# Kernel optimization log

Measured on AMD Instinct MI355X. Metric: run time of the kernel, lower is better.

## Reference

```python
import jax, jax.numpy as jnp
import numpy as np


def setup_inputs() -> dict:
    key = jax.random.key(0)
    k1, k2 = jax.random.split(key)
    B, C, H, W, T = 64, 128, 8, 8, 100
    outputs = jax.random.normal(k1, (B, C, H, W, T), dtype=jnp.float32)
    target = jax.random.uniform(k2, (B, C, H, W, T), dtype=jnp.float32)
    return {"outputs": outputs, "target": target, "n_steps": T, "tau_s": 2}


def _psp(x, tau_s):
    # x: [B, C, H, W, T]; fixed-coefficient leaky integrator over last axis.
    # syn_t = syn_{t-1} * (1 - 1/tau_s) + x_t ; out_t = syn_t / tau_s
    decay = 1.0 - 1.0 / tau_s
    xt = jnp.moveaxis(x, -1, 0)  # [T, B, C, H, W]

    def step(syn, x_t):
        syn = syn * decay + x_t
        return syn, syn / tau_s

    syn0 = jnp.zeros(x.shape[:-1], dtype=x.dtype)
    _, syns = jax.lax.scan(step, syn0, xt)
    return jnp.moveaxis(syns, 0, -1)  # [B, C, H, W, T]


def reference(outputs, target, n_steps, tau_s):
    # n_steps is implied by the trailing axis; kept for signature fidelity.
    target_psp = _psp(target, float(tau_s))
    delta = outputs - target_psp
    return 0.5 * jnp.sum(delta * delta)
```

## Files before the change

kernel.cpp:

```cpp
#include <hip/hip_runtime.h>


constexpr int T    = 100;
constexpr int SEG  = 25;
constexpr int PIX  = 32;
constexpr int TF   = PIX * T;
constexpr int FULL = (TF * 4) / 1024;

typedef const __attribute__((address_space(1))) void* gas_t;
typedef __attribute__((address_space(3))) void*       las_t;

__global__ __launch_bounds__(128) void spike_loss_kernel(
    const float* __restrict__ tgt,
    const float* __restrict__ outs,
    const int*   __restrict__ tau_p,
    float*       __restrict__ out,
    int n_tiles, int tiles_per_block)
{
    __shared__ float lds_t[2][TF];
    __shared__ float lds_o[2][TF];
    __shared__ float ws[2];

    const float tau     = (float)tau_p[0];
    const float inv_tau = 1.0f / tau;
    const float decay   = 1.0f - inv_tau;
    float d25 = 1.0f;
    #pragma unroll
    for (int i = 0; i < SEG; ++i) d25 *= decay;
    const float d50 = d25 * d25;

    const int lane = threadIdx.x & 63;
    const int wv   = threadIdx.x >> 6;

    const int first = blockIdx.x * tiles_per_block;
    int cnt = n_tiles - first;
    if (cnt < 0) cnt = 0;
    if (cnt > tiles_per_block) cnt = tiles_per_block;

    float acc = 0.0f;

    auto stage = [&](int tile, int buf) {
        const float* gt = tgt  + (size_t)tile * TF;
        const float* go = outs + (size_t)tile * TF;
        #pragma unroll
        for (int i = 0; i < FULL / 2; ++i) {
            const int c   = i * 2 + wv;
            const int off = c * 256 + lane * 4;
            __builtin_amdgcn_global_load_lds((gas_t)(gt + off),
                (las_t)&lds_t[buf][c * 256], 16, 0, 0);
            __builtin_amdgcn_global_load_lds((gas_t)(go + off),
                (las_t)&lds_o[buf][c * 256], 16, 0, 0);
        }
        {
            const int off = FULL * 256 + wv * 64 + lane;
            __builtin_amdgcn_global_load_lds((gas_t)(gt + off),
                (las_t)&lds_t[buf][FULL * 256 + wv * 64], 4, 0, 0);
            __builtin_amdgcn_global_load_lds((gas_t)(go + off),
                (las_t)&lds_o[buf][FULL * 256 + wv * 64], 4, 0, 0);
        }
    };

    auto process = [&](int buf) {
        const int p    = threadIdx.x >> 2;
        const int q    = threadIdx.x & 3;
        const int base = p * T + q * SEG;

        float s[SEG];
        float syn = 0.0f;
        #pragma unroll
        for (int i = 0; i < SEG; ++i) {
            syn = fmaf(syn, decay, lds_t[buf][base + i]);
            s[i] = syn;
        }
        const float f1 = __shfl_up(syn, 1, 64);
        const float f2 = __shfl_up(syn, 2, 64);
        const float f3 = __shfl_up(syn, 3, 64);
        float carry = (q >= 1) ? f1 : 0.0f;
        if (q >= 2) carry = fmaf(f2, d25, carry);
        if (q >= 3) carry = fmaf(f3, d50, carry);

        float cp = carry;
        #pragma unroll
        for (int i = 0; i < SEG; ++i) {
            cp *= decay;
            const float st = s[i] + cp;
            const float d  = fmaf(st, -inv_tau, lds_o[buf][base + i]);
            acc = fmaf(d, d, acc);
        }
    };

    if (cnt > 0) stage(first, 0);

    for (int k = 0; k < cnt; ++k) {
        asm volatile("s_waitcnt vmcnt(0)" ::: "memory");
        __syncthreads();
        if (k + 1 < cnt) stage(first + k + 1, (k + 1) & 1);
        process(k & 1);
    }

    #pragma unroll
    for (int off = 32; off > 0; off >>= 1)
        acc += __shfl_down(acc, off, 64);
    if (lane == 0) ws[wv] = acc;
    __syncthreads();
    if (threadIdx.x == 0)
        atomicAdd(out, 0.5f * (ws[0] + ws[1]));
}

extern "C" void kernel_launch(void* const* d_in, const int* in_sizes, int n_in,
                              void* d_out, int out_size, void* d_ws, size_t ws_size,
                              hipStream_t stream) {
    const float* outs = (const float*)d_in[0];
    const float* tgt  = (const float*)d_in[1];
    const int* tau_p  = (const int*)d_in[3];
    float* out        = (float*)d_out;

    const int n_pixels = in_sizes[0] / T;
    const int n_tiles  = n_pixels / PIX;

    const int block = 128;
    const int grid  = 768;
    const int tiles_per_block = (n_tiles + grid - 1) / grid;

    hipMemsetAsync(out, 0, sizeof(float), stream);

    spike_loss_kernel<<<grid, block, 0, stream>>>(
        tgt, outs, tau_p, out, n_tiles, tiles_per_block);
}
```

Measured before the change: 413.3 us.

## Use single-wave blocks, stage only target in LDS, load outputs directly

```diff
diff --git a/kernel.cpp b/kernel.cpp
--- a/kernel.cpp
+++ b/kernel.cpp
@@ -1,25 +1,25 @@
 #include <hip/hip_runtime.h>
 
 
-constexpr int T    = 100;
-constexpr int SEG  = 25;
-constexpr int PIX  = 32;
-constexpr int TF   = PIX * T;
-constexpr int FULL = (TF * 4) / 1024;
+constexpr int T   = 100;
+constexpr int SEG = 25;
+constexpr int PIX = 16;
+constexpr int TF  = PIX * T;
+constexpr int NCH = (TF * 4) / 1024;
+constexpr int NV4 = TF / 4;
 
 typedef const __attribute__((address_space(1))) void* gas_t;
 typedef __attribute__((address_space(3))) void*       las_t;
+typedef float f4 __attribute__((ext_vector_type(4)));
 
-__global__ __launch_bounds__(128) void spike_loss_kernel(
+__global__ __launch_bounds__(64) void spike_loss_kernel(
     const float* __restrict__ tgt,
     const float* __restrict__ outs,
     const int*   __restrict__ tau_p,
     float*       __restrict__ out,
     int n_tiles, int tiles_per_block)
 {
-    __shared__ float lds_t[2][TF];
-    __shared__ float lds_o[2][TF];
-    __shared__ float ws[2];
+    __shared__ __align__(16) float lds_t[2][TF];
 
     const float tau     = (float)tau_p[0];
     const float inv_tau = 1.0f / tau;
@@ -29,40 +29,30 @@
     for (int i = 0; i < SEG; ++i) d25 *= decay;
     const float d50 = d25 * d25;
 
-    const int lane = threadIdx.x & 63;
-    const int wv   = threadIdx.x >> 6;
+    const int tid = threadIdx.x;
 
     const int first = blockIdx.x * tiles_per_block;
     int cnt = n_tiles - first;
     if (cnt < 0) cnt = 0;
     if (cnt > tiles_per_block) cnt = tiles_per_block;
+    if (cnt <= 0) return;
 
     float acc = 0.0f;
 
     auto stage = [&](int tile, int buf) {
-        const float* gt = tgt  + (size_t)tile * TF;
-        const float* go = outs + (size_t)tile * TF;
+        const float* gt = tgt + (size_t)tile * TF;
         #pragma unroll
-        for (int i = 0; i < FULL / 2; ++i) {
-            const int c   = i * 2 + wv;
-            const int off = c * 256 + lane * 4;
-            __builtin_amdgcn_global_load_lds((gas_t)(gt + off),
+        for (int c = 0; c < NCH; ++c) {
+            __builtin_amdgcn_global_load_lds((gas_t)(gt + c * 256 + tid * 4),
                 (las_t)&lds_t[buf][c * 256], 16, 0, 0);
-            __builtin_amdgcn_global_load_lds((gas_t)(go + off),
-                (las_t)&lds_o[buf][c * 256], 16, 0, 0);
         }
-        {
-            const int off = FULL * 256 + wv * 64 + lane;
-            __builtin_amdgcn_global_load_lds((gas_t)(gt + off),
-                (las_t)&lds_t[buf][FULL * 256 + wv * 64], 4, 0, 0);
-            __builtin_amdgcn_global_load_lds((gas_t)(go + off),
-                (las_t)&lds_o[buf][FULL * 256 + wv * 64], 4, 0, 0);
-        }
+        __builtin_amdgcn_global_load_lds((gas_t)(gt + NCH * 256 + tid),
+            (las_t)&lds_t[buf][NCH * 256], 4, 0, 0);
     };
 
     auto process = [&](int buf) {
-        const int p    = threadIdx.x >> 2;
-        const int q    = threadIdx.x & 3;
+        const int p    = tid >> 2;
+        const int q    = tid & 3;
         const int base = p * T + q * SEG;
 
         float s[SEG];
@@ -83,28 +73,56 @@
         #pragma unroll
         for (int i = 0; i < SEG; ++i) {
             cp *= decay;
-            const float st = s[i] + cp;
-            const float d  = fmaf(st, -inv_tau, lds_o[buf][base + i]);
-            acc = fmaf(d, d, acc);
+            lds_t[buf][base + i] = s[i] + cp;
         }
     };
 
-    if (cnt > 0) stage(first, 0);
+    auto pass2 = [&](int tile, int buf) {
+        const f4* o4 = (const f4*)(outs + (size_t)tile * TF);
+        const f4* p4 = (const f4*)lds_t[buf];
+        #pragma unroll
+        for (int j = 0; j < NV4 / 64; ++j) {
+            const int idx = tid + 64 * j;
+            const f4 o = o4[idx];
+            const f4 sy = p4[idx];
+            #pragma unroll
+            for (int c = 0; c < 4; ++c) {
+                const float d = fmaf(sy[c], -inv_tau, o[c]);
+                acc = fmaf(d, d, acc);
+            }
+        }
+        if (tid < NV4 - (NV4 / 64) * 64) {
+            const int idx = (NV4 / 64) * 64 + tid;
+            const f4 o = o4[idx];
+            const f4 sy = p4[idx];
+            #pragma unroll
+            for (int c = 0; c < 4; ++c) {
+                const float d = fmaf(sy[c], -inv_tau, o[c]);
+                acc = fmaf(d, d, acc);
+            }
+        }
+    };
+
+    stage(first, 0);
 
     for (int k = 0; k < cnt; ++k) {
-        asm volatile("s_waitcnt vmcnt(0)" ::: "memory");
-        __syncthreads();
-        if (k + 1 < cnt) stage(first + k + 1, (k + 1) & 1);
+        if (k + 1 < cnt) {
+            stage(first + k + 1, (k + 1) & 1);
+            asm volatile("s_waitcnt vmcnt(7)" ::: "memory");
+        } else {
+            asm volatile("s_waitcnt vmcnt(0)" ::: "memory");
+        }
         process(k & 1);
+        asm volatile("s_waitcnt lgkmcnt(0)" ::: "memory");
+        pass2(first + k, k & 1);
+        asm volatile("s_waitcnt lgkmcnt(0)" ::: "memory");
     }
 
     #pragma unroll
     for (int off = 32; off > 0; off >>= 1)
         acc += __shfl_down(acc, off, 64);
-    if (lane == 0) ws[wv] = acc;
-    __syncthreads();
-    if (threadIdx.x == 0)
-        atomicAdd(out, 0.5f * (ws[0] + ws[1]));
+    if (tid == 0)
+        atomicAdd(out, 0.5f * acc);
 }
 
 extern "C" void kernel_launch(void* const* d_in, const int* in_sizes, int n_in,
@@ -118,8 +136,8 @@
     const int n_pixels = in_sizes[0] / T;
     const int n_tiles  = n_pixels / PIX;
 
-    const int block = 128;
-    const int grid  = 768;
+    const int block = 64;
+    const int grid  = 3072;
     const int tiles_per_block = (n_tiles + grid - 1) / grid;
 
     hipMemsetAsync(out, 0, sizeof(float), stream);
```

Measured after the change: 429.0 us. +3.8%, slower.
